# Kernel tuning notes

Hardware: AMD Instinct MI355X
Metric: run time of the kernel (lower is better)

The kernel has to match this reference:

```python
import jax, jax.numpy as jnp
import numpy as np

EPS = 1e-4  # LayerNorm epsilon from module


def layer_norm(x):
    # torch: (x - mean) / (std + eps), std unbiased (ddof=1), no affine
    mean = jnp.mean(x, axis=-1, keepdims=True)
    std = jnp.sqrt(jnp.var(x, axis=-1, ddof=1, keepdims=True))
    return (x - mean) / (std + EPS)


def setup_inputs() -> dict:
    key = jax.random.key(0)
    ks = jax.random.split(key, 9)
    B, S, D, H, QK = 2, 2048, 1024, 16, 64
    E = D // H  # per-head value/output dim
    scale = 0.02
    x = jax.random.normal(ks[0], (B, S, D), dtype=jnp.float32)
    # stacked per-head projection weights, Linear as x @ W + b
    Wq = jax.random.normal(ks[1], (H, D, QK), dtype=jnp.float32) * scale
    bq = jax.random.normal(ks[2], (H, QK), dtype=jnp.float32) * scale
    Wk = jax.random.normal(ks[3], (H, D, QK), dtype=jnp.float32) * scale
    bk = jax.random.normal(ks[4], (H, QK), dtype=jnp.float32) * scale
    Wv = jax.random.normal(ks[5], (H, D, E), dtype=jnp.float32) * scale
    bv = jax.random.normal(ks[6], (H, E), dtype=jnp.float32) * scale
    Wff = jax.random.normal(ks[7], (D, D), dtype=jnp.float32) * scale
    bff = jax.random.normal(ks[8], (D,), dtype=jnp.float32) * scale
    return {"x": x, "Wq": Wq, "bq": bq, "Wk": Wk, "bk": bk,
            "Wv": Wv, "bv": bv, "Wff": Wff, "bff": bff}


def reference(x, Wq, bq, Wk, bk, Wv, bv, Wff, bff):
    B, S, D = x.shape
    # all heads at once (vectorized over the Python per-head loop)
    Q = jnp.einsum('bsd,hdq->bhsq', x, Wq) + bq[None, :, None, :]
    K = jnp.einsum('bsd,hdq->bhsq', x, Wk) + bk[None, :, None, :]
    V = jnp.einsum('bsd,hde->bhse', x, Wv) + bv[None, :, None, :]
    scores = jnp.einsum('bhsq,bhtq->bhst', Q, K)  # [B,H,S,S]
    # masked_fill on tril(..., diagonal=-1): strictly-lower entries -> -inf
    mask = jnp.tril(jnp.ones((S, S), dtype=bool), k=-1)
    scores = jnp.where(mask[None, None], -jnp.inf, scores)
    # non-standard softmax axis: dim=-2 (over rows s, not keys t)
    attn = jax.nn.softmax(scores, axis=-2)
    heads = jnp.einsum('bhst,bhte->bhse', attn, V)  # [B,H,S,E]
    H, E = heads.shape[1], heads.shape[3]
    combined = heads.transpose(0, 2, 1, 3).reshape(B, S, H * E)  # concat heads
    x = layer_norm(x + combined)
    x = x + (x @ Wff + bff)
    return layer_norm(x)
```

## Files before the change

### kernel.cpp

```cpp
#include <hip/hip_runtime.h>
#include <hip/hip_bf16.h>
#include <math.h>

typedef unsigned short u16;
typedef __attribute__((ext_vector_type(8))) short short8;
typedef __attribute__((ext_vector_type(4))) short short4v;
typedef __attribute__((ext_vector_type(4))) float f32x4;

constexpr int B  = 2;
constexpr int S  = 2048;
constexpr int D  = 1024;
constexpr int H  = 16;
constexpr int DK = 64;
constexpr int BS = B * S;

__device__ __forceinline__ u16 f2b(float f) {
    __hip_bfloat16 h = __float2bfloat16(f);
    return *reinterpret_cast<u16*>(&h);
}
__device__ __forceinline__ float b2f(short s) {
    unsigned int u = ((unsigned int)(u16)s) << 16;
    return __builtin_bit_cast(float, u);
}

#define MFMA16(a, b, c) __builtin_amdgcn_mfma_f32_16x16x32_bf16((a), (b), (c), 0, 0, 0)

__global__ __launch_bounds__(256) void convert_x(const float* __restrict__ src,
                                                 u16* __restrict__ dst)
{
    size_t i = ((size_t)blockIdx.x * 256 + threadIdx.x) * 8;
    f32x4 a = *reinterpret_cast<const f32x4*>(src + i);
    f32x4 b = *reinterpret_cast<const f32x4*>(src + i + 4);
    short8 o;
    o[0] = (short)f2b(a[0]); o[1] = (short)f2b(a[1]);
    o[2] = (short)f2b(a[2]); o[3] = (short)f2b(a[3]);
    o[4] = (short)f2b(b[0]); o[5] = (short)f2b(b[1]);
    o[6] = (short)f2b(b[2]); o[7] = (short)f2b(b[3]);
    *reinterpret_cast<short8*>(dst + i) = o;
}

__global__ __launch_bounds__(256) void tconv(const float* __restrict__ src,
                                             u16* __restrict__ dst, int R, int C)
{
    const int bb = blockIdx.z;
    src += (size_t)bb * R * C;
    dst += (size_t)bb * R * C;
    const int c0 = blockIdx.x * 64, r0 = blockIdx.y * 64;
    __shared__ float Ts[64][65];
    const int tid = threadIdx.x;
    #pragma unroll
    for (int i = 0; i < 4; ++i) {
        int idx = i * 1024 + tid * 4;
        int r = idx >> 6, c = idx & 63;
        f32x4 v = *reinterpret_cast<const f32x4*>(&src[(size_t)(r0 + r) * C + c0 + c]);
        Ts[r][c] = v[0]; Ts[r][c + 1] = v[1]; Ts[r][c + 2] = v[2]; Ts[r][c + 3] = v[3];
    }
    __syncthreads();
    #pragma unroll
    for (int i = 0; i < 4; ++i) {
        int cc = i * 16 + (tid >> 4);
        int rr = (tid & 15) * 4;
        short4v pk;
        pk[0] = (short)f2b(Ts[rr][cc]);     pk[1] = (short)f2b(Ts[rr + 1][cc]);
        pk[2] = (short)f2b(Ts[rr + 2][cc]); pk[3] = (short)f2b(Ts[rr + 3][cc]);
        *reinterpret_cast<short4v*>(&dst[(size_t)(c0 + cc) * R + r0 + rr]) = pk;
    }
}

__global__ __launch_bounds__(256) void qkv_gemm(
    const u16* __restrict__ xb,
    const u16* __restrict__ WqT, const u16* __restrict__ WkT, const u16* __restrict__ WvT,
    const float* __restrict__ bq, const float* __restrict__ bk, const float* __restrict__ bv,
    u16* __restrict__ Qw, u16* __restrict__ Kw, u16* __restrict__ Vtw)
{
    const int id  = blockIdx.x;
    const int m0  = ((id & 7) * 4 + ((id >> 3) & 3)) * 128;
    const int hs  = id >> 5;
    const int h   = hs & 15;
    const int sel = hs >> 4;
    const u16*   WT   = sel == 0 ? WqT : sel == 1 ? WkT : WvT;
    const float* bias = sel == 0 ? bq  : sel == 1 ? bk  : bv;

    __shared__ u16 Xs[128][72];
    __shared__ u16 Ws[64][72];

    const int tid = threadIdx.x;
    const int w = tid >> 6, ln = tid & 15, hi = (tid & 63) >> 4;

    f32x4 acc[2][4];
    #pragma unroll
    for (int m = 0; m < 2; ++m)
        #pragma unroll
        for (int n = 0; n < 4; ++n) acc[m][n] = f32x4{0.f, 0.f, 0.f, 0.f};

    for (int k0 = 0; k0 < D; k0 += 64) {
        #pragma unroll
        for (int i = 0; i < 4; ++i) {
            int ch = i * 256 + tid;
            int r = ch >> 3, c = (ch & 7) * 8;
            *reinterpret_cast<short8*>(&Xs[r][c]) =
                *reinterpret_cast<const short8*>(&xb[(size_t)(m0 + r) * D + k0 + c]);
        }
        #pragma unroll
        for (int i = 0; i < 2; ++i) {
            int ch = i * 256 + tid;
            int r = ch >> 3, c = (ch & 7) * 8;
            *reinterpret_cast<short8*>(&Ws[r][c]) =
                *reinterpret_cast<const short8*>(&WT[((size_t)h * DK + r) * D + k0 + c]);
        }
        __syncthreads();
        #pragma unroll
        for (int ks = 0; ks < 2; ++ks) {
            short8 a[2], bfr[4];
            #pragma unroll
            for (int m = 0; m < 2; ++m)
                a[m] = *reinterpret_cast<const short8*>(&Xs[w * 32 + m * 16 + ln][ks * 32 + hi * 8]);
            #pragma unroll
            for (int n = 0; n < 4; ++n)
                bfr[n] = *reinterpret_cast<const short8*>(&Ws[n * 16 + ln][ks * 32 + hi * 8]);
            #pragma unroll
            for (int m = 0; m < 2; ++m)
                #pragma unroll
                for (int n = 0; n < 4; ++n)
                    acc[m][n] = MFMA16(a[m], bfr[n], acc[m][n]);
        }
        __syncthreads();
    }

    float bv4[4];
    #pragma unroll
    for (int n = 0; n < 4; ++n) bv4[n] = bias[h * DK + n * 16 + ln];

    #pragma unroll
    for (int m = 0; m < 2; ++m)
        #pragma unroll
        for (int n = 0; n < 4; ++n)
            #pragma unroll
            for (int r = 0; r < 4; ++r)
                Xs[w * 32 + m * 16 + hi * 4 + r][n * 16 + ln] =
                    f2b(acc[m][n][r] + bv4[n]);
    __syncthreads();

    const int bidx  = m0 >> 11;
    const int sbase = m0 & 2047;
    if (sel < 2) {
        u16* dst = (sel == 0 ? Qw : Kw) + (size_t)(bidx * H + h) * S * DK;
        #pragma unroll
        for (int i = 0; i < 4; ++i) {
            int ch = i * 256 + tid;
            int r = ch >> 3, c = (ch & 7) * 8;
            *reinterpret_cast<short8*>(&dst[(size_t)(sbase + r) * DK + c]) =
                *reinterpret_cast<const short8*>(&Xs[r][c]);
        }
    } else {
        u16* dst = Vtw + (size_t)(bidx * H + h) * DK * S;
        #pragma unroll
        for (int i = 0; i < 4; ++i) {
            int ch = i * 256 + tid;
            int e = ch >> 4, s8 = (ch & 15) * 8;
            short8 pk;
            #pragma unroll
            for (int j = 0; j < 8; ++j) pk[j] = (short)Xs[s8 + j][e];
            *reinterpret_cast<short8*>(&dst[(size_t)e * S + sbase + s8]) = pk;
        }
    }
}

__global__ __launch_bounds__(256) void col_stats(
    const u16* __restrict__ Qw, const u16* __restrict__ Kw,
    u16* __restrict__ Vtw)
{
    const int id = blockIdx.x;
    const int bh = (id & 7) * 4 + ((id >> 3) & 3);
    const int t0 = (31 - (id >> 5)) * 64;
    const u16* Qh = Qw + (size_t)bh * S * DK;
    const u16* Kh = Kw + (size_t)bh * S * DK;
    u16* Vh = Vtw + (size_t)bh * DK * S;

    __shared__ u16 Qs[2][64][64];
    __shared__ float zbuf[64];

    const int tid = threadIdx.x;
    const int w = tid >> 6, ln = tid & 15, hi = (tid & 63) >> 4;
    const int e0 = tid >> 3, sc = tid & 7;

    char* qb0 = (char*)&Qs[0][0][0];
    char* qb1 = (char*)&Qs[1][0][0];
    auto swz = [](int row, int colb) { return (row * 128 + colb) ^ ((row & 7) << 4); };

    short8 ak[2];
    #pragma unroll
    for (int ks = 0; ks < 2; ++ks)
        ak[ks] = *reinterpret_cast<const short8*>(
            &Kh[(size_t)(t0 + w * 16 + ln) * DK + ks * 32 + hi * 8]);

    float zs[4] = {0.f, 0.f, 0.f, 0.f};

    {
        short8 a = *reinterpret_cast<const short8*>(&Qh[(size_t)e0 * DK + sc * 8]);
        short8 b = *reinterpret_cast<const short8*>(&Qh[(size_t)(e0 + 32) * DK + sc * 8]);
        *reinterpret_cast<short8*>(qb0 + swz(e0, sc * 16)) = a;
        *reinterpret_cast<short8*>(qb0 + swz(e0 + 32, sc * 16)) = b;
    }
    __syncthreads();

    int cur = 0;
    for (int s0b = 0; s0b <= t0; s0b += 64) {
        const bool nxt = (s0b + 64 <= t0);
        short8 nq0, nq1;
        if (nxt) {
            nq0 = *reinterpret_cast<const short8*>(&Qh[(size_t)(s0b + 64 + e0) * DK + sc * 8]);
            nq1 = *reinterpret_cast<const short8*>(&Qh[(size_t)(s0b + 96 + e0) * DK + sc * 8]);
        }
        char* qb = cur ? qb1 : qb0;
        f32x4 c[4];
        #pragma unroll
        for (int n = 0; n < 4; ++n) c[n] = f32x4{0.f, 0.f, 0.f, 0.f};
        #pragma unroll
        for (int ks = 0; ks < 2; ++ks)
            #pragma unroll
            for (int n = 0; n < 4; ++n) {
                short8 bqf = *reinterpret_cast<const short8*>(
                    qb + swz(n * 16 + ln, ks * 64 + hi * 16));
                c[n] = MFMA16(ak[ks], bqf, c[n]);
            }
        if (s0b == t0) {
            #pragma unroll
            for (int n = 0; n < 4; ++n)
                #pragma unroll
                for (int r = 0; r < 4; ++r)
                    if (s0b + n * 16 + ln > t0 + w * 16 + hi * 4 + r)
                        c[n][r] = -INFINITY;
        }
        #pragma unroll
        for (int n = 0; n < 4; ++n)
            #pragma unroll
            for (int r = 0; r < 4; ++r)
                zs[r] += __expf(c[n][r]);
        if (nxt) {
            char* qn = cur ? qb0 : qb1;
            *reinterpret_cast<short8*>(qn + swz(e0, sc * 16)) = nq0;
            *reinterpret_cast<short8*>(qn + swz(e0 + 32, sc * 16)) = nq1;
        }
        __syncthreads();
        cur ^= 1;
    }

    #pragma unroll
    for (int r = 0; r < 4; ++r) {
        #pragma unroll
        for (int msk = 1; msk < 16; msk <<= 1)
            zs[r] += __shfl_xor(zs[r], msk, 64);
    }
    if (ln == 0) {
        #pragma unroll
        for (int r = 0; r < 4; ++r)
            zbuf[w * 16 + hi * 4 + r] = 1.f / zs[r];
    }
    __syncthreads();

    float iz[8];
    #pragma unroll
    for (int j = 0; j < 8; ++j) iz[j] = zbuf[sc * 8 + j];
    #pragma unroll
    for (int pass = 0; pass < 2; ++pass) {
        int e = e0 + 32 * pass;
        u16* vp = &Vh[(size_t)e * S + t0 + sc * 8];
        short8 v = *reinterpret_cast<short8*>(vp);
        short8 o;
        #pragma unroll
        for (int j = 0; j < 8; ++j) o[j] = (short)f2b(b2f(v[j]) * iz[j]);
        *reinterpret_cast<short8*>(vp) = o;
    }
}

__global__ __launch_bounds__(256) void attn_pv(
    const u16* __restrict__ Qw, const u16* __restrict__ Kw, const u16* __restrict__ Vtw,
    float* __restrict__ combined)
{
    const int id = blockIdx.x;
    const int bh = (id & 7) * 4 + ((id >> 3) & 3);
    const int s0 = (id >> 5) * 64;
    const int bidx = bh >> 4, h = bh & 15;
    const u16* Qh = Qw + (size_t)bh * S * DK;
    const u16* Kh = Kw + (size_t)bh * S * DK;
    const u16* Vh = Vtw + (size_t)bh * DK * S;

    __shared__ u16 Vs[2][64][64];
    __shared__ u16 Ps[64][72];

    const int tid = threadIdx.x;
    const int w = tid >> 6, ln = tid & 15, hi = (tid & 63) >> 4;
    const int e0 = tid >> 3, sc = tid & 7;

    char* vb0 = (char*)&Vs[0][0][0];
    char* vb1 = (char*)&Vs[1][0][0];
    auto swz = [](int row, int colb) { return (row * 128 + colb) ^ ((row & 7) << 4); };

    short8 bq[4][2];
    #pragma unroll
    for (int n = 0; n < 4; ++n)
        #pragma unroll
        for (int ks = 0; ks < 2; ++ks)
            bq[n][ks] = *reinterpret_cast<const short8*>(
                &Qh[(size_t)(s0 + n * 16 + ln) * DK + ks * 32 + hi * 8]);

    f32x4 acc[4];
    #pragma unroll
    for (int n = 0; n < 4; ++n) acc[n] = f32x4{0.f, 0.f, 0.f, 0.f};

    {
        short8 a = *reinterpret_cast<const short8*>(&Vh[(size_t)e0 * S + s0 + sc * 8]);
        short8 b = *reinterpret_cast<const short8*>(&Vh[(size_t)(e0 + 32) * S + s0 + sc * 8]);
        *reinterpret_cast<short8*>(vb0 + swz(e0, sc * 16)) = a;
        *reinterpret_cast<short8*>(vb0 + swz(e0 + 32, sc * 16)) = b;
    }

    short8 akA[2], akB[2];
    auto loadK = [&](short8 (&ak)[2], int t1) {
        #pragma unroll
        for (int ks = 0; ks < 2; ++ks)
            ak[ks] = *reinterpret_cast<const short8*>(
                &Kh[(size_t)(t1 + w * 16 + ln) * DK + ks * 32 + hi * 8]);
    };

    loadK(akA, s0);
    __syncthreads();
    int cur = 0;

    auto tile = [&](short8 (&ak)[2], int t1) {
        const bool nxt = (t1 + 64 < S);
        short8 nv0, nv1;
        if (nxt) {
            nv0 = *reinterpret_cast<const short8*>(&Vh[(size_t)e0 * S + t1 + 64 + sc * 8]);
            nv1 = *reinterpret_cast<const short8*>(&Vh[(size_t)(e0 + 32) * S + t1 + 64 + sc * 8]);
        }

        f32x4 st[4];
        #pragma unroll
        for (int n = 0; n < 4; ++n) st[n] = f32x4{0.f, 0.f, 0.f, 0.f};
        #pragma unroll
        for (int ks = 0; ks < 2; ++ks)
            #pragma unroll
            for (int n = 0; n < 4; ++n)
                st[n] = MFMA16(ak[ks], bq[n][ks], st[n]);

        const bool diag = (t1 == s0);
        #pragma unroll
        for (int n = 0; n < 4; ++n) {
            short4v pk;
            #pragma unroll
            for (int r = 0; r < 4; ++r) {
                float p = __expf(st[n][r]);
                if (diag && (s0 + n * 16 + ln) > (t1 + w * 16 + hi * 4 + r)) p = 0.f;
                pk[r] = (short)f2b(p);
            }
            *reinterpret_cast<short4v*>(&Ps[n * 16 + ln][w * 16 + hi * 4]) = pk;
        }
        __syncthreads();

        char* vb = cur ? vb1 : vb0;
        short8 pa[2];
        #pragma unroll
        for (int ks = 0; ks < 2; ++ks)
            pa[ks] = *reinterpret_cast<const short8*>(&Ps[w * 16 + ln][ks * 32 + hi * 8]);
        #pragma unroll
        for (int ks = 0; ks < 2; ++ks)
            #pragma unroll
            for (int n = 0; n < 4; ++n) {
                short8 vv = *reinterpret_cast<const short8*>(
                    vb + swz(n * 16 + ln, ks * 64 + hi * 16));
                acc[n] = MFMA16(pa[ks], vv, acc[n]);
            }

        if (nxt) {
            char* vn = cur ? vb0 : vb1;
            *reinterpret_cast<short8*>(vn + swz(e0, sc * 16)) = nv0;
            *reinterpret_cast<short8*>(vn + swz(e0 + 32, sc * 16)) = nv1;
        }
        __syncthreads();
        cur ^= 1;
    };

    int t1 = s0;
    while (t1 < S) {
        if (t1 + 64 < S) loadK(akB, t1 + 64);
        tile(akA, t1);
        t1 += 64;
        if (t1 >= S) break;
        if (t1 + 64 < S) loadK(akA, t1 + 64);
        tile(akB, t1);
        t1 += 64;
    }

    #pragma unroll
    for (int n = 0; n < 4; ++n)
        #pragma unroll
        for (int r = 0; r < 4; ++r) {
            int s = s0 + w * 16 + hi * 4 + r;
            combined[((size_t)bidx * S + s) * D + h * DK + n * 16 + ln] = acc[n][r];
        }
}

__global__ __launch_bounds__(256) void add_ln(
    const float* __restrict__ a, const float* __restrict__ bsrc,
    float* __restrict__ out, u16* __restrict__ outb)
{
    const int row = blockIdx.x;
    const int tid = threadIdx.x;
    const size_t base = (size_t)row * D;

    float v[4];
    float sum = 0.f;
    #pragma unroll
    for (int i = 0; i < 4; ++i) {
        int c = tid + i * 256;
        float t = a[base + c];
        if (bsrc) t += bsrc[base + c];
        v[i] = t;
        sum += t;
    }

    __shared__ float red[8];
    #pragma unroll
    for (int o = 32; o > 0; o >>= 1) sum += __shfl_down(sum, o, 64);
    const int lane = tid & 63, w = tid >> 6;
    if (lane == 0) red[w] = sum;
    __syncthreads();
    const float mean = (red[0] + red[1] + red[2] + red[3]) * (1.f / D);

    float s2 = 0.f;
    #pragma unroll
    for (int i = 0; i < 4; ++i) { float d2 = v[i] - mean; s2 += d2 * d2; }
    #pragma unroll
    for (int o = 32; o > 0; o >>= 1) s2 += __shfl_down(s2, o, 64);
    if (lane == 0) red[4 + w] = s2;
    __syncthreads();
    const float var = (red[4] + red[5] + red[6] + red[7]) * (1.f / (D - 1));
    const float scale = 1.f / (sqrtf(var) + 1e-4f);

    #pragma unroll
    for (int i = 0; i < 4; ++i) {
        int c = tid + i * 256;
        float o = (v[i] - mean) * scale;
        out[base + c] = o;
        if (outb) outb[base + c] = f2b(o);
    }
}

__global__ __launch_bounds__(256) void ffn(
    const float* __restrict__ x1, const u16* __restrict__ x1b,
    const u16* __restrict__ WffT, const float* __restrict__ bff,
    float* __restrict__ x2)
{
    const int id = blockIdx.x;
    const int m0 = ((id & 7) * 4 + ((id >> 3) & 3)) * 128;
    const int n0 = (id >> 5) * 128;
    __shared__ u16 Xs[128][72];
    __shared__ u16 Ws[128][72];
    const int tid = threadIdx.x;
    const int w = tid >> 6, ln = tid & 15, hi = (tid & 63) >> 4;
    const int wm = w >> 1, wn = w & 1;

    f32x4 acc[4][4];
    #pragma unroll
    for (int m = 0; m < 4; ++m)
        #pragma unroll
        for (int n = 0; n < 4; ++n) acc[m][n] = f32x4{0.f, 0.f, 0.f, 0.f};

    for (int k0 = 0; k0 < D; k0 += 64) {
        #pragma unroll
        for (int i = 0; i < 4; ++i) {
            int ch = i * 256 + tid;
            int r = ch >> 3, c = (ch & 7) * 8;
            *reinterpret_cast<short8*>(&Xs[r][c]) =
                *reinterpret_cast<const short8*>(&x1b[(size_t)(m0 + r) * D + k0 + c]);
            *reinterpret_cast<short8*>(&Ws[r][c]) =
                *reinterpret_cast<const short8*>(&WffT[(size_t)(n0 + r) * D + k0 + c]);
        }
        __syncthreads();
        #pragma unroll
        for (int ks = 0; ks < 2; ++ks) {
            short8 a[4], bb[4];
            #pragma unroll
            for (int m = 0; m < 4; ++m)
                a[m] = *reinterpret_cast<const short8*>(&Xs[wm * 64 + m * 16 + ln][ks * 32 + hi * 8]);
            #pragma unroll
            for (int n = 0; n < 4; ++n)
                bb[n] = *reinterpret_cast<const short8*>(&Ws[wn * 64 + n * 16 + ln][ks * 32 + hi * 8]);
            #pragma unroll
            for (int m = 0; m < 4; ++m)
                #pragma unroll
                for (int n = 0; n < 4; ++n)
                    acc[m][n] = MFMA16(a[m], bb[n], acc[m][n]);
        }
        __syncthreads();
    }

    float bf4[4];
    #pragma unroll
    for (int n = 0; n < 4; ++n) bf4[n] = bff[n0 + wn * 64 + n * 16 + ln];

    #pragma unroll
    for (int m = 0; m < 4; ++m)
        #pragma unroll
        for (int n = 0; n < 4; ++n)
            #pragma unroll
            for (int r = 0; r < 4; ++r) {
                int row = m0 + wm * 64 + m * 16 + hi * 4 + r;
                int col = n0 + wn * 64 + n * 16 + ln;
                size_t idx = (size_t)row * D + col;
                x2[idx] = x1[idx] + acc[m][n][r] + bf4[n];
            }
}

extern "C" void kernel_launch(void* const* d_in, const int* in_sizes, int n_in,
                              void* d_out, int out_size, void* d_ws, size_t ws_size,
                              hipStream_t stream)
{
    const float* x   = (const float*)d_in[0];
    const float* Wq  = (const float*)d_in[1];
    const float* bq  = (const float*)d_in[2];
    const float* Wk  = (const float*)d_in[3];
    const float* bk  = (const float*)d_in[4];
    const float* Wv  = (const float*)d_in[5];
    const float* bv  = (const float*)d_in[6];
    const float* Wff = (const float*)d_in[7];
    const float* bff = (const float*)d_in[8];
    float* out = (float*)d_out;

    const size_t NX = (size_t)BS * D;
    char* p = (char*)d_ws;
    auto alloc = [&](size_t bytes) { char* r = p; p += bytes; return r; };

    u16* xb    = (u16*)alloc(NX * 2);
    u16* WqT   = (u16*)alloc((size_t)H * DK * D * 2);
    u16* WkT   = (u16*)alloc((size_t)H * DK * D * 2);
    u16* WvT   = (u16*)alloc((size_t)H * DK * D * 2);
    u16* WffT  = (u16*)alloc((size_t)D * D * 2);
    u16* Qw    = (u16*)alloc(NX * 2);
    u16* Kw    = (u16*)alloc(NX * 2);
    u16* Vtw   = (u16*)alloc(NX * 2);
    float* combined = (float*)alloc(NX * 4);
    float* x1       = (float*)alloc(NX * 4);
    u16*   x1b = xb;
    float* x2  = (float*)Qw;

    convert_x<<<dim3(NX / 2048), 256, 0, stream>>>(x, xb);
    tconv<<<dim3(1, 16, 16), 256, 0, stream>>>(Wq, WqT, D, DK);
    tconv<<<dim3(1, 16, 16), 256, 0, stream>>>(Wk, WkT, D, DK);
    tconv<<<dim3(1, 16, 16), 256, 0, stream>>>(Wv, WvT, D, DK);
    tconv<<<dim3(16, 16, 1), 256, 0, stream>>>(Wff, WffT, D, D);

    qkv_gemm<<<dim3(1536), 256, 0, stream>>>(
        xb, WqT, WkT, WvT, bq, bk, bv, Qw, Kw, Vtw);

    col_stats<<<dim3(1024), 256, 0, stream>>>(Qw, Kw, Vtw);

    attn_pv<<<dim3(1024), 256, 0, stream>>>(Qw, Kw, Vtw, combined);

    add_ln<<<BS, 256, 0, stream>>>(x, combined, x1, x1b);

    ffn<<<dim3(256), 256, 0, stream>>>(x1, x1b, WffT, bff, x2);

    add_ln<<<BS, 256, 0, stream>>>(x2, nullptr, out, nullptr);
}
```

Before: 164.4 us.

## Retile QKV GEMM to 128x128 with double-buffered swizzled LDS

Fuses the Q, K and V weight matrices into one contiguous transposed buffer so the QKV projection runs as a single GEMM with 128x128 output tiles (two heads per tile) instead of 128x64 per head. The K loop is software-pipelined: global loads for the next K-step go into registers while MFMAs run on the current LDS buffer, with XOR-swizzled LDS layout to avoid bank conflicts. Each wave now holds a 64x64 accumulator, which raises reuse of loaded data but increases register pressure and halves the grid to 768 blocks. The epilogue is also rewritten to stage through swizzled LDS for coalesced Q/K and transposed V stores.

Measured after the change: 157.4 us. -4.3%, faster.

```diff
diff --git a/kernel.cpp b/kernel.cpp
--- a/kernel.cpp
+++ b/kernel.cpp
@@ -68,100 +68,144 @@
 }
 
 __global__ __launch_bounds__(256) void qkv_gemm(
-    const u16* __restrict__ xb,
-    const u16* __restrict__ WqT, const u16* __restrict__ WkT, const u16* __restrict__ WvT,
+    const u16* __restrict__ xb, const u16* __restrict__ WT,
     const float* __restrict__ bq, const float* __restrict__ bk, const float* __restrict__ bv,
     u16* __restrict__ Qw, u16* __restrict__ Kw, u16* __restrict__ Vtw)
 {
-    const int id  = blockIdx.x;
-    const int m0  = ((id & 7) * 4 + ((id >> 3) & 3)) * 128;
-    const int hs  = id >> 5;
-    const int h   = hs & 15;
-    const int sel = hs >> 4;
-    const u16*   WT   = sel == 0 ? WqT : sel == 1 ? WkT : WvT;
-    const float* bias = sel == 0 ? bq  : sel == 1 ? bk  : bv;
-
-    __shared__ u16 Xs[128][72];
-    __shared__ u16 Ws[64][72];
+    const int id   = blockIdx.x;
+    const int xcd  = id & 7;
+    const int j    = id >> 3;
+    const int nblk = xcd * 3 + j % 3;
+    const int mblk = j / 3;
+    const int m0 = mblk * 128, n0 = nblk * 128;
+    const int sel = n0 >> 10;
+    const float* bias = sel == 0 ? bq : sel == 1 ? bk : bv;
+
+    __shared__ u16 SA[2][128][64];
+    __shared__ u16 SB[2][128][64];
 
     const int tid = threadIdx.x;
     const int w = tid >> 6, ln = tid & 15, hi = (tid & 63) >> 4;
-
-    f32x4 acc[2][4];
-    #pragma unroll
-    for (int m = 0; m < 2; ++m)
+    const int wm = w >> 1, wn = w & 1;
+
+    char* a0 = (char*)&SA[0][0][0];
+    char* a1 = (char*)&SA[1][0][0];
+    char* b0 = (char*)&SB[0][0][0];
+    char* b1 = (char*)&SB[1][0][0];
+    auto swz = [](int r, int cb) { return r * 128 + (cb ^ ((r & 7) << 4)); };
+
+    f32x4 acc[4][4];
+    #pragma unroll
+    for (int m = 0; m < 4; ++m)
         #pragma unroll
         for (int n = 0; n < 4; ++n) acc[m][n] = f32x4{0.f, 0.f, 0.f, 0.f};
 
-    for (int k0 = 0; k0 < D; k0 += 64) {
-        #pragma unroll
-        for (int i = 0; i < 4; ++i) {
-            int ch = i * 256 + tid;
-            int r = ch >> 3, c = (ch & 7) * 8;
-            *reinterpret_cast<short8*>(&Xs[r][c]) =
-                *reinterpret_cast<const short8*>(&xb[(size_t)(m0 + r) * D + k0 + c]);
-        }
-        #pragma unroll
-        for (int i = 0; i < 2; ++i) {
-            int ch = i * 256 + tid;
-            int r = ch >> 3, c = (ch & 7) * 8;
-            *reinterpret_cast<short8*>(&Ws[r][c]) =
-                *reinterpret_cast<const short8*>(&WT[((size_t)h * DK + r) * D + k0 + c]);
-        }
-        __syncthreads();
+    short8 ra[4], rb[4];
+    auto stageLoad = [&](int k0) {
+        #pragma unroll
+        for (int c = 0; c < 4; ++c) {
+            int idx = c * 256 + tid, r = idx >> 3, col = (idx & 7) * 8;
+            ra[c] = *reinterpret_cast<const short8*>(&xb[(size_t)(m0 + r) * D + k0 + col]);
+            rb[c] = *reinterpret_cast<const short8*>(&WT[(size_t)(n0 + r) * D + k0 + col]);
+        }
+    };
+    auto stageWrite = [&](char* abuf, char* bbuf) {
+        #pragma unroll
+        for (int c = 0; c < 4; ++c) {
+            int idx = c * 256 + tid, r = idx >> 3, cb = (idx & 7) * 16;
+            *reinterpret_cast<short8*>(abuf + swz(r, cb)) = ra[c];
+            *reinterpret_cast<short8*>(bbuf + swz(r, cb)) = rb[c];
+        }
+    };
+
+    stageLoad(0);
+    stageWrite(a0, b0);
+    __syncthreads();
+
+    int cur = 0;
+    for (int it = 0; it < 16; ++it) {
+        const bool nxt = (it + 1 < 16);
+        if (nxt) stageLoad((it + 1) * 64);
+        char* ac = cur ? a1 : a0;
+        char* bc = cur ? b1 : b0;
         #pragma unroll
         for (int ks = 0; ks < 2; ++ks) {
-            short8 a[2], bfr[4];
-            #pragma unroll
-            for (int m = 0; m < 2; ++m)
-                a[m] = *reinterpret_cast<const short8*>(&Xs[w * 32 + m * 16 + ln][ks * 32 + hi * 8]);
+            short8 af[4], bf[4];
+            #pragma unroll
+            for (int m = 0; m < 4; ++m)
+                af[m] = *reinterpret_cast<const short8*>(
+                    ac + swz(wm * 64 + m * 16 + ln, ks * 64 + hi * 16));
             #pragma unroll
             for (int n = 0; n < 4; ++n)
-                bfr[n] = *reinterpret_cast<const short8*>(&Ws[n * 16 + ln][ks * 32 + hi * 8]);
-            #pragma unroll
-            for (int m = 0; m < 2; ++m)
+                bf[n] = *reinterpret_cast<const short8*>(
+                    bc + swz(wn * 64 + n * 16 + ln, ks * 64 + hi * 16));
+            #pragma unroll
+            for (int m = 0; m < 4; ++m)
                 #pragma unroll
                 for (int n = 0; n < 4; ++n)
-                    acc[m][n] = MFMA16(a[m], bfr[n], acc[m][n]);
-        }
-        __syncthreads();
-    }
-
-    float bv4[4];
-    #pragma unroll
-    for (int n = 0; n < 4; ++n) bv4[n] = bias[h * DK + n * 16 + ln];
-
-    #pragma unroll
-    for (int m = 0; m < 2; ++m)
-        #pragma unroll
-        for (int n = 0; n < 4; ++n)
-            #pragma unroll
-            for (int r = 0; r < 4; ++r)
-                Xs[w * 32 + m * 16 + hi * 4 + r][n * 16 + ln] =
-                    f2b(acc[m][n][r] + bv4[n]);
-    __syncthreads();
-
+                    acc[m][n] = MFMA16(af[m], bf[n], acc[m][n]);
+        }
+        if (nxt) stageWrite(cur ? a0 : a1, cur ? b0 : b1);
+        __syncthreads();
+        cur ^= 1;
+    }
+
+    float bias4[4];
+    #pragma unroll
+    for (int n = 0; n < 4; ++n)
+        bias4[n] = bias[(n0 & 1023) + wn * 64 + n * 16 + ln];
+
+    char* eb = a0;
     const int bidx  = m0 >> 11;
     const int sbase = m0 & 2047;
+    const int h0    = (n0 & 1023) >> 6;
+
     if (sel < 2) {
-        u16* dst = (sel == 0 ? Qw : Kw) + (size_t)(bidx * H + h) * S * DK;
-        #pragma unroll
-        for (int i = 0; i < 4; ++i) {
-            int ch = i * 256 + tid;
-            int r = ch >> 3, c = (ch & 7) * 8;
-            *reinterpret_cast<short8*>(&dst[(size_t)(sbase + r) * DK + c]) =
-                *reinterpret_cast<const short8*>(&Xs[r][c]);
+        #pragma unroll
+        for (int m = 0; m < 4; ++m)
+            #pragma unroll
+            for (int n = 0; n < 4; ++n)
+                #pragma unroll
+                for (int r = 0; r < 4; ++r) {
+                    int row = wm * 64 + m * 16 + hi * 4 + r;
+                    int col = wn * 64 + n * 16 + ln;
+                    *reinterpret_cast<u16*>(eb + row * 256 + ((col * 2) ^ ((row & 7) << 4))) =
+                        f2b(acc[m][n][r] + bias4[n]);
+                }
+        __syncthreads();
+        u16* dst0 = sel == 0 ? Qw : Kw;
+        #pragma unroll
+        for (int c = 0; c < 8; ++c) {
+            int idx = c * 256 + tid;
+            int row = idx >> 4, g = idx & 15;
+            short8 v = *reinterpret_cast<const short8*>(
+                eb + row * 256 + ((g * 16) ^ ((row & 7) << 4)));
+            int h = h0 + (g >> 3), j0 = (g & 7) * 8;
+            *reinterpret_cast<short8*>(
+                &dst0[((size_t)(bidx * H + h) * S + sbase + row) * DK + j0]) = v;
         }
     } else {
-        u16* dst = Vtw + (size_t)(bidx * H + h) * DK * S;
-        #pragma unroll
-        for (int i = 0; i < 4; ++i) {
-            int ch = i * 256 + tid;
-            int e = ch >> 4, s8 = (ch & 15) * 8;
-            short8 pk;
-            #pragma unroll
-            for (int j = 0; j < 8; ++j) pk[j] = (short)Xs[s8 + j][e];
-            *reinterpret_cast<short8*>(&dst[(size_t)e * S + sbase + s8]) = pk;
+        #pragma unroll
+        for (int m = 0; m < 4; ++m)
+            #pragma unroll
+            for (int n = 0; n < 4; ++n)
+                #pragma unroll
+                for (int r = 0; r < 4; ++r) {
+                    int row = wm * 64 + m * 16 + hi * 4 + r;
+                    int col = wn * 64 + n * 16 + ln;
+                    *reinterpret_cast<u16*>(eb + col * 256 + ((row * 2) ^ ((col & 7) << 4))) =
+                        f2b(acc[m][n][r] + bias4[n]);
+                }
+        __syncthreads();
+        #pragma unroll
+        for (int c = 0; c < 8; ++c) {
+            int idx = c * 256 + tid;
+            int e = idx >> 4, g = idx & 15;
+            short8 v = *reinterpret_cast<const short8*>(
+                eb + e * 256 + ((g * 16) ^ ((e & 7) << 4)));
+            int h = h0 + (e >> 6), ein = e & 63;
+            *reinterpret_cast<short8*>(
+                &Vtw[((size_t)(bidx * H + h) * DK + ein) * S + sbase + g * 8]) = v;
         }
     }
 }
@@ -534,9 +578,7 @@
     auto alloc = [&](size_t bytes) { char* r = p; p += bytes; return r; };
 
     u16* xb    = (u16*)alloc(NX * 2);
-    u16* WqT   = (u16*)alloc((size_t)H * DK * D * 2);
-    u16* WkT   = (u16*)alloc((size_t)H * DK * D * 2);
-    u16* WvT   = (u16*)alloc((size_t)H * DK * D * 2);
+    u16* WT    = (u16*)alloc((size_t)3 * H * DK * D * 2);
     u16* WffT  = (u16*)alloc((size_t)D * D * 2);
     u16* Qw    = (u16*)alloc(NX * 2);
     u16* Kw    = (u16*)alloc(NX * 2);
@@ -547,13 +589,13 @@
     float* x2  = (float*)Qw;
 
     convert_x<<<dim3(NX / 2048), 256, 0, stream>>>(x, xb);
-    tconv<<<dim3(1, 16, 16), 256, 0, stream>>>(Wq, WqT, D, DK);
-    tconv<<<dim3(1, 16, 16), 256, 0, stream>>>(Wk, WkT, D, DK);
-    tconv<<<dim3(1, 16, 16), 256, 0, stream>>>(Wv, WvT, D, DK);
+    tconv<<<dim3(1, 16, 16), 256, 0, stream>>>(Wq, WT, D, DK);
+    tconv<<<dim3(1, 16, 16), 256, 0, stream>>>(Wk, WT + (size_t)H * DK * D, D, DK);
+    tconv<<<dim3(1, 16, 16), 256, 0, stream>>>(Wv, WT + (size_t)2 * H * DK * D, D, DK);
     tconv<<<dim3(16, 16, 1), 256, 0, stream>>>(Wff, WffT, D, D);
 
-    qkv_gemm<<<dim3(1536), 256, 0, stream>>>(
-        xb, WqT, WkT, WvT, bq, bk, bv, Qw, Kw, Vtw);
+    qkv_gemm<<<dim3(768), 256, 0, stream>>>(
+        xb, WT, bq, bk, bv, Qw, Kw, Vtw);
 
     col_stats<<<dim3(1024), 256, 0, stream>>>(Qw, Kw, Vtw);
 
```
